# Kernel optimization log

Measured on AMD Instinct MI355X. Metric: run time of the kernel, lower is better.

Reference implementation:

```python
import jax, jax.numpy as jnp
import numpy as np

K = 4        # Legendre orders / channels
T = 1024     # sequence length (== max_len)
B = 2        # batch
D = 256      # feature dim
THETA = 200.0  # LegT window length; dt = 1/theta


def _make_hippo_legt(N):
    # A_{nk} = -sqrt((2n+1)(2k+1)) * sigma_{nk}; B_n = sqrt(2n+1)
    n = np.arange(N, dtype=np.float64)
    P = np.sqrt(2.0 * n + 1.0)
    PP = P[:, None] * P[None, :]
    diff = n[:, None] - n[None, :]
    sign = np.ones_like(PP)
    upper = diff < 0
    sign[upper] = (-1.0) ** (-diff[upper])
    A = -PP * sign
    Bv = P.reshape(N, 1)
    return A, Bv


def _legt_kernel(T_, N, theta):
    """M[k] = Abar^k @ Bbar, k = 0..T-1 (bilinear discretization, dt=1/theta)."""
    A, Bv = _make_hippo_legt(N)
    dt = 1.0 / float(theta)
    I = np.eye(N)
    inv = np.linalg.inv(I - 0.5 * dt * A)
    Abar = inv @ (I + 0.5 * dt * A)
    Bbar = (inv @ (Bv * dt)).squeeze(-1)
    M = np.zeros((T_, N), dtype=np.float64)
    cur = Bbar.copy()
    for k in range(T_):
        M[k] = cur
        cur = Abar @ cur
    return M.astype(np.float32)


def setup_inputs() -> dict:
    key = jax.random.key(0)
    h = jax.random.normal(key, (B, T, D), dtype=jnp.float32)
    M = jnp.asarray(_legt_kernel(T, K, THETA))  # (T, K) precomputed buffer
    return {"h": h, "M": M}


def reference(h, M):
    # c[b, t, k, d] = sum_{s<=t} M[t-s, k] * h[b, s, d]
    B_, T_, d = h.shape
    t = jnp.arange(T_)
    ix = t[:, None] - t[None, :]                    # (T, T)
    mask = (ix >= 0).astype(h.dtype)
    W = M[jnp.clip(ix, 0)] * mask[:, :, None]       # (T, T, K) causal Toeplitz bank
    return jnp.einsum('tsk,bsd->btkd', W, h)        # (B, T, K, D)
```

## Files before the change

kernel.cpp:

```cpp
#include <hip/hip_runtime.h>
#include <math.h>

namespace {

constexpr int K_ = 4;
constexpr int T_ = 1024;
constexpr int B_ = 2;
constexpr int D_ = 256;
constexpr int NSEQ = B_ * D_;

constexpr int CH = 128;
constexpr int L_ = T_ / CH;
constexpr int LOG_CH = 7;

__device__ __forceinline__ void base_consts(float Af[4][4], float Bf[4]) {
    const double dt = 1.0 / 200.0;
    double P[4], A[4][4];
#pragma unroll
    for (int n = 0; n < 4; ++n) P[n] = sqrt(2.0 * n + 1.0);
#pragma unroll
    for (int n = 0; n < 4; ++n)
#pragma unroll
        for (int k = 0; k < 4; ++k) {
            double s = (n >= k) ? 1.0 : (((k - n) & 1) ? -1.0 : 1.0);
            A[n][k] = -P[n] * P[k] * s;
        }
    double aug[4][9];
#pragma unroll
    for (int r = 0; r < 4; ++r) {
#pragma unroll
        for (int c = 0; c < 4; ++c) {
            double idc = (r == c) ? 1.0 : 0.0;
            aug[r][c]     = idc - 0.5 * dt * A[r][c];
            aug[r][4 + c] = idc + 0.5 * dt * A[r][c];
        }
        aug[r][8] = P[r] * dt;
    }
#pragma unroll
    for (int p = 0; p < 4; ++p) {
        double pinv = 1.0 / aug[p][p];
#pragma unroll
        for (int c = 0; c < 9; ++c) aug[p][c] *= pinv;
#pragma unroll
        for (int r = 0; r < 4; ++r) {
            if (r == p) continue;
            double f = aug[r][p];
#pragma unroll
            for (int c = 0; c < 9; ++c) aug[r][c] -= f * aug[p][c];
        }
    }
#pragma unroll
    for (int r = 0; r < 4; ++r) {
#pragma unroll
        for (int c = 0; c < 4; ++c) Af[r][c] = (float)aug[r][4 + c];
        Bf[r] = (float)aug[r][8];
    }
}

__device__ __forceinline__ void matsq(const float X[4][4], float Y[4][4]) {
#pragma unroll
    for (int r = 0; r < 4; ++r)
#pragma unroll
        for (int c = 0; c < 4; ++c) {
            float acc = 0.f;
#pragma unroll
            for (int k = 0; k < 4; ++k) acc = fmaf(X[r][k], X[k][c], acc);
            Y[r][c] = acc;
        }
}

__device__ __forceinline__ void scan_consts(float AP[LOG_CH][4][4]) {
    float Af[4][4], Bf[4];
    base_consts(Af, Bf);
    float X[4][4], Y[4][4];
    matsq(Af, X);
    matsq(X, Y);
    matsq(Y, X);
#pragma unroll
    for (int s = 0; s < LOG_CH; ++s) {
#pragma unroll
        for (int r = 0; r < 4; ++r)
#pragma unroll
            for (int c = 0; c < 4; ++c) AP[s][r][c] = X[r][c];
        matsq(X, Y);
#pragma unroll
        for (int r = 0; r < 4; ++r)
#pragma unroll
            for (int c = 0; c < 4; ++c) X[r][c] = Y[r][c];
    }
}

__global__ __launch_bounds__(256) void k1a_chunk_states(
    const float* __restrict__ h, const float* __restrict__ M,
    float* __restrict__ ws_y)
{
    const int dlane = threadIdx.x & 63;
    const int csub  = threadIdx.x >> 6;
    const int sg    = blockIdx.x & 7;
    const int cg    = blockIdx.x >> 3;
    const int seq = sg * 64 + dlane;
    const int b = seq >> 8, d = seq & (D_ - 1);
    const int c = cg * 4 + csub;

    const float* hp = h + ((size_t)(b * T_ + c * L_)) * D_ + d;
    float y0 = 0.f, y1 = 0.f, y2 = 0.f, y3 = 0.f;
#pragma unroll
    for (int i = 0; i < L_; ++i) {
        float hv = hp[i * D_];
        const float* mr = M + (L_ - 1 - i) * K_;
        y0 = fmaf(mr[0], hv, y0);
        y1 = fmaf(mr[1], hv, y1);
        y2 = fmaf(mr[2], hv, y2);
        y3 = fmaf(mr[3], hv, y3);
    }
    float4* wp = (float4*)ws_y + (size_t)c * NSEQ + seq;
    *wp = make_float4(y0, y1, y2, y3);
}

__global__ __launch_bounds__(256) void k1b_scan(
    const float* __restrict__ ws_y, float* __restrict__ ws_init)
{
    const int sp = threadIdx.x & 1;
    const int c  = threadIdx.x >> 1;
    const int seq = blockIdx.x * 2 + sp;

    float AP[LOG_CH][4][4];
    scan_consts(AP);

    float4 v = ((const float4*)ws_y)[(size_t)c * NSEQ + seq];

    __shared__ float4 lds[CH * 2];
#pragma unroll
    for (int s = 0; s < LOG_CH; ++s) {
        const int off = 1 << s;
        lds[threadIdx.x] = v;
        __syncthreads();
        if (c >= off) {
            float4 p = lds[threadIdx.x - off * 2];
            v.x = fmaf(AP[s][0][0], p.x, fmaf(AP[s][0][1], p.y, fmaf(AP[s][0][2], p.z, fmaf(AP[s][0][3], p.w, v.x))));
            v.y = fmaf(AP[s][1][0], p.x, fmaf(AP[s][1][1], p.y, fmaf(AP[s][1][2], p.z, fmaf(AP[s][1][3], p.w, v.y))));
            v.z = fmaf(AP[s][2][0], p.x, fmaf(AP[s][2][1], p.y, fmaf(AP[s][2][2], p.z, fmaf(AP[s][2][3], p.w, v.z))));
            v.w = fmaf(AP[s][3][0], p.x, fmaf(AP[s][3][1], p.y, fmaf(AP[s][3][2], p.z, fmaf(AP[s][3][3], p.w, v.w))));
        }
        __syncthreads();
    }
    float4* ip = (float4*)ws_init;
    if (c < CH - 1) ip[(size_t)(c + 1) * NSEQ + seq] = v;
    if (c == 0)     ip[seq] = make_float4(0.f, 0.f, 0.f, 0.f);
}

__global__ __launch_bounds__(256) void k2_emit(
    const float* __restrict__ h, const float* __restrict__ ws_init,
    float* __restrict__ out)
{
    const int d = threadIdx.x;
    const int c = blockIdx.x & (CH - 1);
    const int b = blockIdx.x >> LOG_CH;

    float Af[4][4], Bf[4];
    base_consts(Af, Bf);

    float4 xi = ((const float4*)ws_init)[(size_t)c * NSEQ + b * D_ + d];
    float x0 = xi.x, x1 = xi.y, x2 = xi.z, x3 = xi.w;

    const float* hp = h + ((size_t)(b * T_ + c * L_)) * D_ + d;
    float* op = out + ((size_t)(b * T_ + c * L_)) * K_ * D_ + d;
#pragma unroll
    for (int i = 0; i < L_; ++i) {
        float hv = hp[i * D_];
        float n0 = fmaf(Af[0][0], x0, fmaf(Af[0][1], x1, fmaf(Af[0][2], x2, fmaf(Af[0][3], x3, Bf[0] * hv))));
        float n1 = fmaf(Af[1][0], x0, fmaf(Af[1][1], x1, fmaf(Af[1][2], x2, fmaf(Af[1][3], x3, Bf[1] * hv))));
        float n2 = fmaf(Af[2][0], x0, fmaf(Af[2][1], x1, fmaf(Af[2][2], x2, fmaf(Af[2][3], x3, Bf[2] * hv))));
        float n3 = fmaf(Af[3][0], x0, fmaf(Af[3][1], x1, fmaf(Af[3][2], x2, fmaf(Af[3][3], x3, Bf[3] * hv))));
        x0 = n0; x1 = n1; x2 = n2; x3 = n3;
        op[0 * D_] = x0; op[1 * D_] = x1; op[2 * D_] = x2; op[3 * D_] = x3;
        op += K_ * D_;
    }
}

}

extern "C" void kernel_launch(void* const* d_in, const int* in_sizes, int n_in,
                              void* d_out, int out_size, void* d_ws, size_t ws_size,
                              hipStream_t stream) {
    const float* h = (const float*)d_in[0];
    const float* M = (const float*)d_in[1];
    float* out = (float*)d_out;

    float* ws_y    = (float*)d_ws;
    float* ws_init = ws_y + (size_t)CH * NSEQ * K_;

    k1a_chunk_states<<<(NSEQ / 64) * (CH / 4), 256, 0, stream>>>(h, M, ws_y);
    k1b_scan<<<NSEQ / 2, 256, 0, stream>>>(ws_y, ws_init);
    k2_emit<<<B_ * CH, 256, 0, stream>>>(h, ws_init, out);
}
```

Before: 63.49 us.

## Fuse chunk-state computation into scan kernel and use nontemporal output stores

Merges the per-chunk state reduction kernel into the scan kernel, so each scan thread computes its own chunk contribution directly from h. This removes one kernel launch and the workspace write/read of the chunk states. The trade-off is that the h reads in the fused kernel are poorly coalesced, because adjacent threads map to different chunks. Separately, output stores in the emit kernel become nontemporal to avoid polluting the cache.

```diff
diff --git a/kernel.cpp b/kernel.cpp
--- a/kernel.cpp
+++ b/kernel.cpp
@@ -90,17 +90,17 @@
     }
 }
 
-__global__ __launch_bounds__(256) void k1a_chunk_states(
+__global__ __launch_bounds__(256) void k_scan(
     const float* __restrict__ h, const float* __restrict__ M,
-    float* __restrict__ ws_y)
+    float* __restrict__ ws_init)
 {
-    const int dlane = threadIdx.x & 63;
-    const int csub  = threadIdx.x >> 6;
-    const int sg    = blockIdx.x & 7;
-    const int cg    = blockIdx.x >> 3;
-    const int seq = sg * 64 + dlane;
+    const int sp = threadIdx.x & 1;
+    const int c  = threadIdx.x >> 1;
+    const int seq = blockIdx.x * 2 + sp;
     const int b = seq >> 8, d = seq & (D_ - 1);
-    const int c = cg * 4 + csub;
+
+    float AP[LOG_CH][4][4];
+    scan_consts(AP);
 
     const float* hp = h + ((size_t)(b * T_ + c * L_)) * D_ + d;
     float y0 = 0.f, y1 = 0.f, y2 = 0.f, y3 = 0.f;
@@ -113,21 +113,7 @@
         y2 = fmaf(mr[2], hv, y2);
         y3 = fmaf(mr[3], hv, y3);
     }
-    float4* wp = (float4*)ws_y + (size_t)c * NSEQ + seq;
-    *wp = make_float4(y0, y1, y2, y3);
-}
-
-__global__ __launch_bounds__(256) void k1b_scan(
-    const float* __restrict__ ws_y, float* __restrict__ ws_init)
-{
-    const int sp = threadIdx.x & 1;
-    const int c  = threadIdx.x >> 1;
-    const int seq = blockIdx.x * 2 + sp;
-
-    float AP[LOG_CH][4][4];
-    scan_consts(AP);
-
-    float4 v = ((const float4*)ws_y)[(size_t)c * NSEQ + seq];
+    float4 v = make_float4(y0, y1, y2, y3);
 
     __shared__ float4 lds[CH * 2];
 #pragma unroll
@@ -149,7 +135,7 @@
     if (c == 0)     ip[seq] = make_float4(0.f, 0.f, 0.f, 0.f);
 }
 
-__global__ __launch_bounds__(256) void k2_emit(
+__global__ __launch_bounds__(256) void k_emit(
     const float* __restrict__ h, const float* __restrict__ ws_init,
     float* __restrict__ out)
 {
@@ -173,7 +159,10 @@
         float n2 = fmaf(Af[2][0], x0, fmaf(Af[2][1], x1, fmaf(Af[2][2], x2, fmaf(Af[2][3], x3, Bf[2] * hv))));
         float n3 = fmaf(Af[3][0], x0, fmaf(Af[3][1], x1, fmaf(Af[3][2], x2, fmaf(Af[3][3], x3, Bf[3] * hv))));
         x0 = n0; x1 = n1; x2 = n2; x3 = n3;
-        op[0 * D_] = x0; op[1 * D_] = x1; op[2 * D_] = x2; op[3 * D_] = x3;
+        __builtin_nontemporal_store(x0, &op[0 * D_]);
+        __builtin_nontemporal_store(x1, &op[1 * D_]);
+        __builtin_nontemporal_store(x2, &op[2 * D_]);
+        __builtin_nontemporal_store(x3, &op[3 * D_]);
         op += K_ * D_;
     }
 }
@@ -187,10 +176,8 @@
     const float* M = (const float*)d_in[1];
     float* out = (float*)d_out;
 
-    float* ws_y    = (float*)d_ws;
-    float* ws_init = ws_y + (size_t)CH * NSEQ * K_;
+    float* ws_init = (float*)d_ws;
 
-    k1a_chunk_states<<<(NSEQ / 64) * (CH / 4), 256, 0, stream>>>(h, M, ws_y);
-    k1b_scan<<<NSEQ / 2, 256, 0, stream>>>(ws_y, ws_init);
-    k2_emit<<<B_ * CH, 256, 0, stream>>>(h, ws_init, out);
+    k_scan<<<NSEQ / 2, 256, 0, stream>>>(h, M, ws_init);
+    k_emit<<<B_ * CH, 256, 0, stream>>>(h, ws_init, out);
 }
```

After: 63.86 us. No clear change (+0.6%).
